# Optimization experiments

Hardware: AMD Instinct MI355X
Metric: run time of the kernel (lower is better)

Reference implementation:

```python
import jax, jax.numpy as jnp
import numpy as np

EPS = 1e-5
GROUPS = 32


def group_norm(x, gamma, beta):
    b, c, h, w = x.shape
    xg = x.reshape(b, GROUPS, c // GROUPS, h, w)
    mu = xg.mean(axis=(2, 3, 4), keepdims=True)
    var = xg.var(axis=(2, 3, 4), keepdims=True)
    xn = ((xg - mu) * jax.lax.rsqrt(var + EPS)).reshape(b, c, h, w)
    return xn * gamma[None, :, None, None] + beta[None, :, None, None]


def setup_inputs() -> dict:
    key = jax.random.key(0)
    ks = jax.random.split(key, 4)
    b, c, h, w = 4, 512, 64, 64
    x = jax.random.normal(ks[0], (b, c, h, w), dtype=jnp.float32)
    gn_w = jnp.ones((c,), jnp.float32)
    gn_b = jnp.zeros((c,), jnp.float32)
    qkv_w = jax.random.normal(ks[1], (3 * c, c), dtype=jnp.float32) * (c ** -0.5)
    qkv_b = jnp.zeros((3 * c,), jnp.float32)
    out_w = jax.random.normal(ks[2], (c, c), dtype=jnp.float32) * (c ** -0.5)
    out_b = jnp.zeros((c,), jnp.float32)
    return {"x": x, "gn_w": gn_w, "gn_b": gn_b, "qkv_w": qkv_w,
            "qkv_b": qkv_b, "out_w": out_w, "out_b": out_b}


def reference(x, gn_w, gn_b, qkv_w, qkv_b, out_w, out_b):
    b, c, hh, ww = x.shape
    n = hh * ww
    h = group_norm(x, gn_w, gn_b)
    # 1x1 conv == per-pixel matmul over channels
    qkv = jnp.einsum('bchw,oc->bohw', h, qkv_w) + qkv_b[None, :, None, None]
    q, k, v = jnp.split(qkv, 3, axis=1)
    q = q.transpose(0, 2, 3, 1).reshape(b, n, c)   # (b, n, c)
    k = k.reshape(b, c, n)                          # (b, c, n)
    v = v.transpose(0, 2, 3, 1).reshape(b, n, c)   # (b, n, c)
    attn = jax.nn.softmax(jnp.einsum('bnc,bcm->bnm', q, k) * (c ** -0.5), axis=-1)
    out = jnp.einsum('bnm,bmc->bnc', attn, v)
    out = out.reshape(b, hh, ww, c).transpose(0, 3, 1, 2)
    out = jnp.einsum('bchw,oc->bohw', out, out_w) + out_b[None, :, None, None]
    return out + x
```

## Files before the change

### kernel.cpp

```cpp
#include <hip/hip_runtime.h>
#include <cmath>

#define NB 4
#define NC 512
#define NN 4096
#define ATTN_SCALE 0.04419417382415922f

typedef __bf16 bf16x8 __attribute__((ext_vector_type(8)));
typedef float floatx4 __attribute__((ext_vector_type(4)));

__device__ __forceinline__ unsigned short f2bf(float f) {
    union { float f; unsigned int u; } v; v.f = f;
    return (unsigned short)((v.u + 0x7fffu + ((v.u >> 16) & 1u)) >> 16);
}
__device__ __forceinline__ unsigned short f2bf_trunc(float f) {
    union { float f; unsigned int u; } v; v.f = f;
    return (unsigned short)(v.u >> 16);
}
__device__ __forceinline__ float bf2f(unsigned short u) {
    union { unsigned int u; float f; } v; v.u = ((unsigned int)u) << 16;
    return v.f;
}

__device__ __forceinline__ void gload_lds16(const unsigned short* gp, unsigned short* lp) {
    __builtin_amdgcn_global_load_lds(
        (const __attribute__((address_space(1))) void*)gp,
        (__attribute__((address_space(3))) void*)lp, 16, 0, 0);
}

__global__ __launch_bounds__(256) void gn_partial_kernel(
    const float* __restrict__ x, float* __restrict__ part)
{
    int blk = blockIdx.x;
    int bg = blk >> 3, sub = blk & 7;
    const float4* xv = (const float4*)(x + (size_t)bg * 16 * NN + (size_t)sub * 8192);
    float s1 = 0.f, s2 = 0.f;
#pragma unroll
    for (int i = 0; i < 8; ++i) {
        float4 v = xv[threadIdx.x + i * 256];
        s1 += v.x + v.y + v.z + v.w;
        s2 += v.x * v.x + v.y * v.y + v.z * v.z + v.w * v.w;
    }
#pragma unroll
    for (int off = 32; off; off >>= 1) {
        s1 += __shfl_xor(s1, off, 64);
        s2 += __shfl_xor(s2, off, 64);
    }
    __shared__ float r1[4], r2[4];
    int lane = threadIdx.x & 63, w = threadIdx.x >> 6;
    if (lane == 0) { r1[w] = s1; r2[w] = s2; }
    __syncthreads();
    if (threadIdx.x == 0) {
        part[blk * 2]     = r1[0] + r1[1] + r1[2] + r1[3];
        part[blk * 2 + 1] = r2[0] + r2[1] + r2[2] + r2[3];
    }
}

__global__ __launch_bounds__(128) void gn_final_kernel(
    const float* __restrict__ part, const float* __restrict__ gw,
    const float* __restrict__ gb, float* __restrict__ ss)
{
    int tg = threadIdx.x;
    int b = tg >> 5, g = tg & 31;
    float s1 = 0.f, s2 = 0.f;
#pragma unroll
    for (int s = 0; s < 8; ++s) {
        s1 += part[(tg * 8 + s) * 2];
        s2 += part[(tg * 8 + s) * 2 + 1];
    }
    float mean = s1 * (1.0f / 65536.0f);
    float var  = s2 * (1.0f / 65536.0f) - mean * mean;
    float rstd = rsqrtf(var + 1e-5f);
#pragma unroll
    for (int i = 0; i < 16; ++i) {
        int c = g * 16 + i;
        float sc = rstd * gw[c];
        ss[b * NC + c] = sc;
        ss[2048 + b * NC + c] = gb[c] - mean * sc;
    }
}

__global__ __launch_bounds__(256) void wconv_kernel(
    const float* __restrict__ qkv_w, const float* __restrict__ out_w,
    unsigned short* __restrict__ wq, unsigned short* __restrict__ wo)
{
    int i = blockIdx.x * 256 + threadIdx.x;
    const int NQ = 1536 * 512;
    if (i < NQ) wq[i] = f2bf(qkv_w[i]);
    else        wo[i - NQ] = f2bf(out_w[i - NQ]);
}

__global__ __launch_bounds__(256) void htnorm_kernel(
    const float* __restrict__ x, const float* __restrict__ ss,
    unsigned short* __restrict__ ht)
{
    int b = blockIdx.z;
    int c0 = blockIdx.y * 32, n0 = blockIdx.x * 32;
    __shared__ float T[32][33];
    int tx = threadIdx.x & 31, ty = threadIdx.x >> 5;
    const float* xb = x + ((size_t)b * NC + c0) * NN;
    const float* sc = ss + b * NC + c0;
    const float* sh = ss + 2048 + b * NC + c0;
#pragma unroll
    for (int i = 0; i < 4; ++i) {
        int c = ty + i * 8;
        T[c][tx] = xb[(size_t)c * NN + n0 + tx] * sc[c] + sh[c];
    }
    __syncthreads();
    unsigned short* hb = ht + ((size_t)b * NN + n0) * NC + c0;
#pragma unroll
    for (int i = 0; i < 4; ++i) {
        int n = ty + i * 8;
        hb[(size_t)n * NC + tx] = f2bf(T[tx][n]);
    }
}

template<int MODE, int BM, int BN, int MINB>
__global__ __launch_bounds__(256, MINB) void mfma_gemm(
    const unsigned short* __restrict__ Abase,
    const unsigned short* __restrict__ Bbase,
    const float* __restrict__ e0, const float* __restrict__ e1,
    float* __restrict__ outf,
    unsigned short* __restrict__ ob0, unsigned short* __restrict__ ob1)
{
    constexpr int K = 512;
    constexpr int NT = K / 32;
    constexpr int FI = BM / 32;
    constexpr int FJ = BN / 32;
    const int z = blockIdx.z;
    const size_t bnc = (size_t)NN * NC;
    const size_t bss = (size_t)NN * NN;

    const unsigned short* A;
    const unsigned short* B;
    if constexpr (MODE == 0)      { A = Abase + (size_t)z * bnc; B = Bbase; }
    else if constexpr (MODE == 1) { A = Abase; B = Bbase + (size_t)z * bnc; }
    else if constexpr (MODE == 2) { A = Abase + (size_t)z * bnc; B = Bbase + (size_t)z * bnc; }
    else                          { A = Abase; B = Bbase + (size_t)z * bnc; }

    const int m0 = blockIdx.y * BM;
    const int n0 = blockIdx.x * BN;

    __shared__ __attribute__((aligned(16))) unsigned short As[2][BM * 32];
    __shared__ __attribute__((aligned(16))) unsigned short Bs[2][BN * 32];

    const int t = threadIdx.x;
    const int lane = t & 63;
    const int w = t >> 6;
    const int wr = w >> 1, wc = w & 1;

    const int sr = w * 16 + (lane >> 2);
    const int scs = ((lane & 3) ^ ((lane >> 3) & 3)) * 8;
    const int lds_elem = w * 512;
    const int kslot = lane >> 4;

    floatx4 acc[FI][FJ] = {};

    auto stage = [&](int buf, int k0) {
#pragma unroll
        for (int s = 0; s < BM / 64; ++s)
            gload_lds16(A + (size_t)(m0 + s * 64 + sr) * K + k0 + scs,
                        &As[buf][s * 2048 + lds_elem]);
#pragma unroll
        for (int s = 0; s < BN / 64; ++s)
            gload_lds16(B + (size_t)(n0 + s * 64 + sr) * K + k0 + scs,
                        &Bs[buf][s * 2048 + lds_elem]);
    };

    auto compute = [&](int buf) {
        bf16x8 af[FI], bfr[FJ];
#pragma unroll
        for (int i = 0; i < FI; ++i) {
            const int ra = wr * (BM / 2) + i * 16 + (lane & 15);
            af[i] = *(const bf16x8*)(&As[buf][ra * 32 + ((kslot ^ ((ra >> 1) & 3)) * 8)]);
        }
#pragma unroll
        for (int j = 0; j < FJ; ++j) {
            const int rb = wc * (BN / 2) + j * 16 + (lane & 15);
            bfr[j] = *(const bf16x8*)(&Bs[buf][rb * 32 + ((kslot ^ ((rb >> 1) & 3)) * 8)]);
        }
#pragma unroll
        for (int i = 0; i < FI; ++i)
#pragma unroll
            for (int j = 0; j < FJ; ++j)
                acc[i][j] = __builtin_amdgcn_mfma_f32_16x16x32_bf16(
                    af[i], bfr[j], acc[i][j], 0, 0, 0);
    };

    stage(0, 0);
    asm volatile("s_waitcnt vmcnt(0)" ::: "memory");
    __syncthreads();
    int cur = 0;
    for (int kt = 0; kt < NT - 1; ++kt) {
        stage(cur ^ 1, (kt + 1) * 32);
        compute(cur);
        asm volatile("s_waitcnt vmcnt(0)" ::: "memory");
        __syncthreads();
        cur ^= 1;
    }
    compute(cur);

    const int fr = lane >> 4;
    const int fc = lane & 15;

    if constexpr (MODE == 2) {
        float rs[FI][4];
#pragma unroll
        for (int i = 0; i < FI; ++i)
#pragma unroll
            for (int r = 0; r < 4; ++r) rs[i][r] = 0.f;
#pragma unroll
        for (int i = 0; i < FI; ++i) {
#pragma unroll
            for (int j = 0; j < FJ; ++j) {
                int n = n0 + wc * (BN / 2) + j * 16 + fc;
                int mbase = m0 + wr * (BM / 2) + i * 16 + fr * 4;
#pragma unroll
                for (int r = 0; r < 4; ++r) {
                    float e = __expf(acc[i][j][r]);
                    ob0[(size_t)z * bss + (size_t)(mbase + r) * NN + n] = f2bf_trunc(e);
                    rs[i][r] += e;
                }
            }
        }
#pragma unroll
        for (int i = 0; i < FI; ++i) {
#pragma unroll
            for (int r = 0; r < 4; ++r) {
                float v = rs[i][r];
                v += __shfl_xor(v, 1, 16);
                v += __shfl_xor(v, 2, 16);
                v += __shfl_xor(v, 4, 16);
                v += __shfl_xor(v, 8, 16);
                if (fc == 0) {
                    int m = m0 + wr * (BM / 2) + i * 16 + fr * 4 + r;
                    atomicAdd(&outf[z * NN + m], v);
                }
            }
        }
        return;
    }

#pragma unroll
    for (int i = 0; i < FI; ++i) {
#pragma unroll
        for (int j = 0; j < FJ; ++j) {
            int n = n0 + wc * (BN / 2) + j * 16 + fc;
            int mbase = m0 + wr * (BM / 2) + i * 16 + fr * 4;
#pragma unroll
            for (int r = 0; r < 4; ++r) {
                int m = mbase + r;
                float val = acc[i][j][r];
                if constexpr (MODE == 0) {
                    val += e0[n];
                    if (n < 512) ob0[((size_t)z * NN + m) * NC + n] = f2bf(val * ATTN_SCALE);
                    else         ob1[((size_t)z * NN + m) * NC + (n - 512)] = f2bf(val);
                } else if constexpr (MODE == 1) {
                    val += e0[1024 + m];
                    ob0[((size_t)z * NC + m) * NN + n] = f2bf(val);
                } else {
                    size_t idx = ((size_t)z * NC + m) * NN + n;
                    outf[idx] = val + e0[m] + e1[idx];
                }
            }
        }
    }
}

__global__ __launch_bounds__(256, 4) void pv_gemm(
    const unsigned short* __restrict__ Abase,
    const unsigned short* __restrict__ Bbase,
    const float* __restrict__ L,
    unsigned short* __restrict__ Ob)
{
    const int id = blockIdx.x;
    const int xcd = id & 7;
    const int j0 = id >> 3;
    const int ct = j0 & 3;
    const int pairl = j0 >> 2;
    const int p = pairl * 8 + xcd;
    const int ptile = p & 63, z = p >> 6;

    const size_t bss = (size_t)NN * NN, bnc = (size_t)NN * NC;
    const unsigned short* A = Abase + (size_t)z * bss;
    const unsigned short* B = Bbase + (size_t)z * bnc;
    const int m0 = ptile * 64;
    const int n0 = ct * 128;

    __shared__ __attribute__((aligned(16))) unsigned short As[64 * 64];
    __shared__ __attribute__((aligned(16))) unsigned short Bs[128 * 64];

    const int t = threadIdx.x;
    const int lane = t & 63;
    const int w = t >> 6;
    const int wr = w >> 1, wc = w & 1;

    const int sr = w * 8 + (lane >> 3);
    const int scs = ((lane & 7) ^ (lane >> 3)) * 8;
    const int lds_elem = w * 512;

    floatx4 acc[2][4] = {};

    for (int k0 = 0; k0 < NN; k0 += 64) {
#pragma unroll
        for (int s = 0; s < 2; ++s)
            gload_lds16(A + (size_t)(m0 + s * 32 + sr) * NN + k0 + scs,
                        As + s * 2048 + lds_elem);
#pragma unroll
        for (int s = 0; s < 4; ++s)
            gload_lds16(B + (size_t)(n0 + s * 32 + sr) * NN + k0 + scs,
                        Bs + s * 2048 + lds_elem);
        __syncthreads();

        bf16x8 af[2][2], bfr[4][2];
#pragma unroll
        for (int i = 0; i < 2; ++i) {
            const int ra = wr * 32 + i * 16 + (lane & 15);
#pragma unroll
            for (int kk = 0; kk < 2; ++kk)
                af[i][kk] = *(const bf16x8*)(As + ra * 64 +
                    (((kk * 4 + (lane >> 4)) ^ (ra & 7)) * 8));
        }
#pragma unroll
        for (int jj = 0; jj < 4; ++jj) {
            const int rb = wc * 64 + jj * 16 + (lane & 15);
#pragma unroll
            for (int kk = 0; kk < 2; ++kk)
                bfr[jj][kk] = *(const bf16x8*)(Bs + rb * 64 +
                    (((kk * 4 + (lane >> 4)) ^ (rb & 7)) * 8));
        }
#pragma unroll
        for (int kk = 0; kk < 2; ++kk)
#pragma unroll
            for (int i = 0; i < 2; ++i)
#pragma unroll
                for (int jj = 0; jj < 4; ++jj)
                    acc[i][jj] = __builtin_amdgcn_mfma_f32_16x16x32_bf16(
                        af[i][kk], bfr[jj][kk], acc[i][jj], 0, 0, 0);
        __syncthreads();
    }

    const int fr = lane >> 4;
    const int fc = lane & 15;
#pragma unroll
    for (int i = 0; i < 2; ++i) {
#pragma unroll
        for (int r = 0; r < 4; ++r) {
            int m = m0 + wr * 32 + i * 16 + fr * 4 + r;
            float linv = 1.0f / L[z * NN + m];
#pragma unroll
            for (int jj = 0; jj < 4; ++jj) {
                int n = n0 + wc * 64 + jj * 16 + fc;
                Ob[(size_t)z * bnc + (size_t)m * NC + n] = f2bf(acc[i][jj][r] * linv);
            }
        }
    }
}

extern "C" void kernel_launch(void* const* d_in, const int* in_sizes, int n_in,
                              void* d_out, int out_size, void* d_ws, size_t ws_size,
                              hipStream_t stream)
{
    const float* x     = (const float*)d_in[0];
    const float* gn_w  = (const float*)d_in[1];
    const float* gn_b  = (const float*)d_in[2];
    const float* qkv_w = (const float*)d_in[3];
    const float* qkv_b = (const float*)d_in[4];
    const float* out_w = (const float*)d_in[5];
    const float* out_b = (const float*)d_in[6];
    float* out = (float*)d_out;

    const size_t bnc = (size_t)NN * NC;
    char* w = (char*)d_ws;
    float* ss   = (float*)w;                 w += 16384;
    float* part = (float*)w;                 w += 8192;
    float* Lsum = (float*)w;                 w += (size_t)NB * NN * 4;
    unsigned short* wq = (unsigned short*)w; w += (size_t)1536 * 512 * 2;
    unsigned short* wo = (unsigned short*)w; w += (size_t)512 * 512 * 2;
    unsigned short* qt = (unsigned short*)w; w += NB * bnc * 2;
    unsigned short* kt = (unsigned short*)w; w += NB * bnc * 2;
    unsigned short* vt = (unsigned short*)w; w += NB * bnc * 2;
    unsigned short* SP = (unsigned short*)w; w += (size_t)NB * NN * NN * 2;
    unsigned short* ht = SP;
    unsigned short* Ob = qt;

    hipMemsetAsync(Lsum, 0, (size_t)NB * NN * sizeof(float), stream);

    gn_partial_kernel<<<1024, 256, 0, stream>>>(x, part);
    gn_final_kernel<<<1, 128, 0, stream>>>(part, gn_w, gn_b, ss);
    wconv_kernel<<<(1536 * 512 + 512 * 512) / 256, 256, 0, stream>>>(qkv_w, out_w, wq, wo);
    htnorm_kernel<<<dim3(NN / 32, NC / 32, NB), 256, 0, stream>>>(x, ss, ht);

    mfma_gemm<0, 128, 128, 3><<<dim3(1024 / 128, NN / 128, NB), 256, 0, stream>>>(
        ht, wq, qkv_b, nullptr, nullptr, qt, kt);
    mfma_gemm<1, 64, 128, 4><<<dim3(NN / 128, 512 / 64, NB), 256, 0, stream>>>(
        wq + (size_t)1024 * 512, ht, qkv_b, nullptr, nullptr, vt, nullptr);

    mfma_gemm<2, 128, 128, 3><<<dim3(NN / 128, NN / 128, NB), 256, 0, stream>>>(
        qt, kt, nullptr, nullptr, Lsum, SP, nullptr);
    pv_gemm<<<dim3(1024), 256, 0, stream>>>(SP, vt, Lsum, Ob);

    mfma_gemm<4, 64, 128, 4><<<dim3(NN / 128, 512 / 64, NB), 256, 0, stream>>>(
        wo, Ob, out_b, x, out, nullptr, nullptr);
}
```

Before: 377.6 us.

## Add triple-buffered GEMM pipeline and dedicated QK^T kernel with XCD-aware tiling

Generalizes the mfma_gemm mainloop to a configurable multi-buffer pipeline (3 buffers) with partial vmcnt waits, so global-to-LDS loads run further ahead of the MFMA compute. The QK^T+exp stage moves into a new qk_gemm kernel that uses K-tiles of 64 with a wider swizzle and a 1D grid remapped across XCDs for L2 locality. The aim is to hide load latency and cut barrier count per K. In exchange it uses more LDS per block, which may lower occupancy.

```diff
diff --git a/kernel.cpp b/kernel.cpp
--- a/kernel.cpp
+++ b/kernel.cpp
@@ -17,15 +17,18 @@
     union { float f; unsigned int u; } v; v.f = f;
     return (unsigned short)(v.u >> 16);
 }
-__device__ __forceinline__ float bf2f(unsigned short u) {
-    union { unsigned int u; float f; } v; v.u = ((unsigned int)u) << 16;
-    return v.f;
-}
 
 __device__ __forceinline__ void gload_lds16(const unsigned short* gp, unsigned short* lp) {
     __builtin_amdgcn_global_load_lds(
         (const __attribute__((address_space(1))) void*)gp,
         (__attribute__((address_space(3))) void*)lp, 16, 0, 0);
+}
+
+template<int N> __device__ __forceinline__ void wait_vmcnt() {
+    if constexpr (N == 0) asm volatile("s_waitcnt vmcnt(0)" ::: "memory");
+    else if constexpr (N == 3) asm volatile("s_waitcnt vmcnt(3)" ::: "memory");
+    else if constexpr (N == 4) asm volatile("s_waitcnt vmcnt(4)" ::: "memory");
+    else if constexpr (N == 6) asm volatile("s_waitcnt vmcnt(6)" ::: "memory");
 }
 
 __global__ __launch_bounds__(256) void gn_partial_kernel(
@@ -115,7 +118,7 @@
     }
 }
 
-template<int MODE, int BM, int BN, int MINB>
+template<int MODE, int BM, int BN, int KD, int NBUF, int MINB>
 __global__ __launch_bounds__(256, MINB) void mfma_gemm(
     const unsigned short* __restrict__ Abase,
     const unsigned short* __restrict__ Bbase,
@@ -123,26 +126,25 @@
     float* __restrict__ outf,
     unsigned short* __restrict__ ob0, unsigned short* __restrict__ ob1)
 {
-    constexpr int K = 512;
-    constexpr int NT = K / 32;
+    constexpr int NT = KD / 32;
     constexpr int FI = BM / 32;
     constexpr int FJ = BN / 32;
+    constexpr int LPS = BM / 64 + BN / 64;
+    constexpr int DEPTH = NBUF - 1;
+    const size_t bnc = (size_t)NN * NC;
+
     const int z = blockIdx.z;
-    const size_t bnc = (size_t)NN * NC;
-    const size_t bss = (size_t)NN * NN;
+    const int m0 = blockIdx.y * BM;
+    const int n0 = blockIdx.x * BN;
 
     const unsigned short* A;
     const unsigned short* B;
     if constexpr (MODE == 0)      { A = Abase + (size_t)z * bnc; B = Bbase; }
     else if constexpr (MODE == 1) { A = Abase; B = Bbase + (size_t)z * bnc; }
-    else if constexpr (MODE == 2) { A = Abase + (size_t)z * bnc; B = Bbase + (size_t)z * bnc; }
     else                          { A = Abase; B = Bbase + (size_t)z * bnc; }
 
-    const int m0 = blockIdx.y * BM;
-    const int n0 = blockIdx.x * BN;
-
-    __shared__ __attribute__((aligned(16))) unsigned short As[2][BM * 32];
-    __shared__ __attribute__((aligned(16))) unsigned short Bs[2][BN * 32];
+    __shared__ __attribute__((aligned(16))) unsigned short As[NBUF][BM * 32];
+    __shared__ __attribute__((aligned(16))) unsigned short Bs[NBUF][BN * 32];
 
     const int t = threadIdx.x;
     const int lane = t & 63;
@@ -156,14 +158,15 @@
 
     floatx4 acc[FI][FJ] = {};
 
-    auto stage = [&](int buf, int k0) {
+    auto stage = [&](int buf, int tile) {
+        const int k0 = tile * 32;
 #pragma unroll
         for (int s = 0; s < BM / 64; ++s)
-            gload_lds16(A + (size_t)(m0 + s * 64 + sr) * K + k0 + scs,
+            gload_lds16(A + (size_t)(m0 + s * 64 + sr) * KD + k0 + scs,
                         &As[buf][s * 2048 + lds_elem]);
 #pragma unroll
         for (int s = 0; s < BN / 64; ++s)
-            gload_lds16(B + (size_t)(n0 + s * 64 + sr) * K + k0 + scs,
+            gload_lds16(B + (size_t)(n0 + s * 64 + sr) * KD + k0 + scs,
                         &Bs[buf][s * 2048 + lds_elem]);
     };
 
@@ -187,59 +190,28 @@
                     af[i], bfr[j], acc[i][j], 0, 0, 0);
     };
 
-    stage(0, 0);
-    asm volatile("s_waitcnt vmcnt(0)" ::: "memory");
-    __syncthreads();
-    int cur = 0;
-    for (int kt = 0; kt < NT - 1; ++kt) {
-        stage(cur ^ 1, (kt + 1) * 32);
-        compute(cur);
-        asm volatile("s_waitcnt vmcnt(0)" ::: "memory");
-        __syncthreads();
-        cur ^= 1;
-    }
-    compute(cur);
+#pragma unroll
+    for (int d = 0; d < DEPTH; ++d) stage(d, d);
+    wait_vmcnt<(DEPTH - 1) * LPS>();
+    __builtin_amdgcn_s_barrier();
+
+#pragma unroll
+    for (int kt = 0; kt < NT - DEPTH; ++kt) {
+        stage((kt + DEPTH) % NBUF, kt + DEPTH);
+        compute(kt % NBUF);
+        asm volatile("s_waitcnt lgkmcnt(0)" ::: "memory");
+        wait_vmcnt<(DEPTH - 1) * LPS>();
+        __builtin_amdgcn_s_barrier();
+    }
+
+    compute((NT - 2) % NBUF);
+    asm volatile("s_waitcnt lgkmcnt(0)" ::: "memory");
+    wait_vmcnt<0>();
+    __builtin_amdgcn_s_barrier();
+    compute((NT - 1) % NBUF);
 
     const int fr = lane >> 4;
     const int fc = lane & 15;
-
-    if constexpr (MODE == 2) {
-        float rs[FI][4];
-#pragma unroll
-        for (int i = 0; i < FI; ++i)
-#pragma unroll
-            for (int r = 0; r < 4; ++r) rs[i][r] = 0.f;
-#pragma unroll
-        for (int i = 0; i < FI; ++i) {
-#pragma unroll
-            for (int j = 0; j < FJ; ++j) {
-                int n = n0 + wc * (BN / 2) + j * 16 + fc;
-                int mbase = m0 + wr * (BM / 2) + i * 16 + fr * 4;
-#pragma unroll
-                for (int r = 0; r < 4; ++r) {
-                    float e = __expf(acc[i][j][r]);
-                    ob0[(size_t)z * bss + (size_t)(mbase + r) * NN + n] = f2bf_trunc(e);
-                    rs[i][r] += e;
-                }
-            }
-        }
-#pragma unroll
-        for (int i = 0; i < FI; ++i) {
-#pragma unroll
-            for (int r = 0; r < 4; ++r) {
-                float v = rs[i][r];
-                v += __shfl_xor(v, 1, 16);
-                v += __shfl_xor(v, 2, 16);
-                v += __shfl_xor(v, 4, 16);
-                v += __shfl_xor(v, 8, 16);
-                if (fc == 0) {
-                    int m = m0 + wr * (BM / 2) + i * 16 + fr * 4 + r;
-                    atomicAdd(&outf[z * NN + m], v);
-                }
-            }
-        }
-        return;
-    }
 
 #pragma unroll
     for (int i = 0; i < FI; ++i) {
@@ -267,6 +239,122 @@
     }
 }
 
+__global__ __launch_bounds__(256, 2) void qk_gemm(
+    const unsigned short* __restrict__ qt,
+    const unsigned short* __restrict__ kt,
+    float* __restrict__ Lsum,
+    unsigned short* __restrict__ SP)
+{
+    const int id = blockIdx.x;
+    const int xcd = id & 7, j = id >> 3;
+    const int row = xcd * 16 + (j & 15);
+    const int z = row >> 5;
+    const int m0 = (row & 31) * 128;
+    const int n0 = (j >> 4) * 128;
+
+    const size_t bnc = (size_t)NN * NC, bss = (size_t)NN * NN;
+    const unsigned short* A = qt + (size_t)z * bnc;
+    const unsigned short* B = kt + (size_t)z * bnc;
+
+    __shared__ __attribute__((aligned(16))) unsigned short As[2][128 * 64];
+    __shared__ __attribute__((aligned(16))) unsigned short Bs[2][128 * 64];
+
+    const int t = threadIdx.x, lane = t & 63, w = t >> 6;
+    const int wr = w >> 1, wc = w & 1;
+
+    const int sra = t >> 3;
+    const int scs = ((t & 7) ^ (sra & 7)) * 8;
+    const int sdst = t * 8;
+
+    floatx4 acc[4][4] = {};
+
+    auto stage = [&](int buf, int k0) {
+#pragma unroll
+        for (int s = 0; s < 4; ++s)
+            gload_lds16(A + (size_t)(m0 + s * 32 + sra) * 512 + k0 + scs,
+                        &As[buf][s * 2048 + sdst]);
+#pragma unroll
+        for (int s = 0; s < 4; ++s)
+            gload_lds16(B + (size_t)(n0 + s * 32 + sra) * 512 + k0 + scs,
+                        &Bs[buf][s * 2048 + sdst]);
+    };
+
+    auto compute = [&](int buf) {
+#pragma unroll
+        for (int kk = 0; kk < 2; ++kk) {
+            bf16x8 af[4], bfr[4];
+#pragma unroll
+            for (int i = 0; i < 4; ++i) {
+                const int ra = wr * 64 + i * 16 + (lane & 15);
+                af[i] = *(const bf16x8*)(&As[buf][ra * 64 +
+                        (((kk * 4 + (lane >> 4)) ^ (ra & 7)) * 8)]);
+            }
+#pragma unroll
+            for (int jf = 0; jf < 4; ++jf) {
+                const int rb = wc * 64 + jf * 16 + (lane & 15);
+                bfr[jf] = *(const bf16x8*)(&Bs[buf][rb * 64 +
+                        (((kk * 4 + (lane >> 4)) ^ (rb & 7)) * 8)]);
+            }
+#pragma unroll
+            for (int i = 0; i < 4; ++i)
+#pragma unroll
+                for (int jf = 0; jf < 4; ++jf)
+                    acc[i][jf] = __builtin_amdgcn_mfma_f32_16x16x32_bf16(
+                        af[i], bfr[jf], acc[i][jf], 0, 0, 0);
+        }
+    };
+
+    stage(0, 0);
+    asm volatile("s_waitcnt vmcnt(0)" ::: "memory");
+    __builtin_amdgcn_s_barrier();
+#pragma unroll
+    for (int kt = 0; kt < 7; ++kt) {
+        stage((kt + 1) & 1, (kt + 1) * 64);
+        compute(kt & 1);
+        asm volatile("s_waitcnt lgkmcnt(0)" ::: "memory");
+        asm volatile("s_waitcnt vmcnt(0)" ::: "memory");
+        __builtin_amdgcn_s_barrier();
+    }
+    compute(1);
+
+    const int fr = lane >> 4;
+    const int fc = lane & 15;
+    float rs[4][4];
+#pragma unroll
+    for (int i = 0; i < 4; ++i)
+#pragma unroll
+        for (int r = 0; r < 4; ++r) rs[i][r] = 0.f;
+#pragma unroll
+    for (int i = 0; i < 4; ++i) {
+#pragma unroll
+        for (int jf = 0; jf < 4; ++jf) {
+            int n = n0 + wc * 64 + jf * 16 + fc;
+            int mbase = m0 + wr * 64 + i * 16 + fr * 4;
+#pragma unroll
+            for (int r = 0; r < 4; ++r) {
+                float e = __expf(acc[i][jf][r]);
+                SP[(size_t)z * bss + (size_t)(mbase + r) * NN + n] = f2bf_trunc(e);
+                rs[i][r] += e;
+            }
+        }
+    }
+#pragma unroll
+    for (int i = 0; i < 4; ++i) {
+#pragma unroll
+        for (int r = 0; r < 4; ++r) {
+            float v = rs[i][r];
+            v += __shfl_xor(v, 1, 16);
+            v += __shfl_xor(v, 2, 16);
+            v += __shfl_xor(v, 4, 16);
+            v += __shfl_xor(v, 8, 16);
+            if (fc == 0) {
+                int m = m0 + wr * 64 + i * 16 + fr * 4 + r;
+                atomicAdd(&Lsum[z * NN + m], v);
+            }
+        }
+    }
+}
+
 __global__ __launch_bounds__(256, 4) void pv_gemm(
     const unsigned short* __restrict__ Abase,
     const unsigned short* __restrict__ Bbase,
@@ -391,15 +479,14 @@
     wconv_kernel<<<(1536 * 512 + 512 * 512) / 256, 256, 0, stream>>>(qkv_w, out_w, wq, wo);
     htnorm_kernel<<<dim3(NN / 32, NC / 32, NB), 256, 0, stream>>>(x, ss, ht);
 
-    mfma_gemm<0, 128, 128, 3><<<dim3(1024 / 128, NN / 128, NB), 256, 0, stream>>>(
+    mfma_gemm<0, 128, 128, 512, 3, 3><<<dim3(1024 / 128, NN / 128, NB), 256, 0, stream>>>(
         ht, wq, qkv_b, nullptr, nullptr, qt, kt);
-    mfma_gemm<1, 64, 128, 4><<<dim3(NN / 128, 512 / 64, NB), 256, 0, stream>>>(
+    mfma_gemm<1, 64, 128, 512, 3, 4><<<dim3(NN / 128, 512 / 64, NB), 256, 0, stream>>>(
         wq + (size_t)1024 * 512, ht, qkv_b, nullptr, nullptr, vt, nullptr);
 
-    mfma_gemm<2, 128, 128, 3><<<dim3(NN / 128, NN / 128, NB), 256, 0, stream>>>(
-        qt, kt, nullptr, nullptr, Lsum, SP, nullptr);
+    qk_gemm<<<dim3(4096), 256, 0, stream>>>(qt, kt, Lsum, SP);
     pv_gemm<<<dim3(1024), 256, 0, stream>>>(SP, vt, Lsum, Ob);
 
-    mfma_gemm<4, 64, 128, 4><<<dim3(NN / 128, 512 / 64, NB), 256, 0, stream>>>(
+    mfma_gemm<4, 64, 128, 512, 3, 4><<<dim3(NN / 128, 512 / 64, NB), 256, 0, stream>>>(
         wo, Ob, out_b, x, out, nullptr, nullptr);
 }
```

Result: faster. 369.4 us (-2.2%).
